# Kernel tuning notes

Hardware: AMD Instinct MI355X
Metric: run time of the kernel (lower is better)

Reference implementation:

```python
import jax, jax.numpy as jnp
import numpy as np

NUM_HEADS = 4
NUM_POINTS = 8


def setup_inputs() -> dict:
    key0 = jax.random.key(0)
    ks = jax.random.split(key0, 14)
    B, S, N, D, C = 1, 6, 10000, 4, 128
    Hf, Wf = 46, 80
    M = Hf * Wf
    HP2 = NUM_HEADS * NUM_POINTS * 2
    HP = NUM_HEADS * NUM_POINTS
    inp = {
        "query": jax.random.normal(ks[0], (B, N, C), jnp.float32),
        "key": jax.random.normal(ks[1], (S, M, B, C), jnp.float32),
        "value": jax.random.normal(ks[2], (S, M, B, C), jnp.float32),
        "query_pos": jax.random.normal(ks[3], (B, N, C), jnp.float32),
        "reference_points_cam": jax.random.uniform(ks[4], (S, B, N, D, 2), jnp.float32),
        "Wv": jax.random.normal(ks[5], (C, C), jnp.float32) * 0.02,
        "bv": jnp.zeros((C,), jnp.float32),
        "Wo": jax.random.normal(ks[6], (C, HP2), jnp.float32) * 0.02,
        "bo": jax.random.normal(ks[7], (HP2,), jnp.float32) * 0.5,
        "Wa": jax.random.normal(ks[8], (C, HP), jnp.float32) * 0.02,
        "ba": jnp.zeros((HP,), jnp.float32),
        "Wp": jax.random.normal(ks[9], (C, C), jnp.float32) * 0.02,
        "bp": jnp.zeros((C,), jnp.float32),
        "spatial_shapes": np.array([[Hf, Wf]], dtype=np.int64),
        "bev_mask": jax.random.uniform(ks[10], (S, B, N, D)) < 0.3,
    }
    return inp


def _bilinear_sample(value_hw, loc, Hf, Wf):
    # value_hw: [BS, H, Hf*Wf, Dh]; loc: [BS, L, H, P, 2] normalized to [0,1]
    # grid_sample(align_corners=False, padding=zeros) semantics: ix = x*W - 0.5
    x = loc[..., 0] * Wf - 0.5
    y = loc[..., 1] * Hf - 0.5
    x0 = jnp.floor(x)
    y0 = jnp.floor(y)
    lx = x - x0
    ly = y - y0
    x0i = x0.astype(jnp.int32)
    y0i = y0.astype(jnp.int32)

    BS, L, H, P = x.shape
    Dh = value_hw.shape[-1]

    def gat(xi, yi):
        valid = (xi >= 0) & (xi < Wf) & (yi >= 0) & (yi < Hf)
        idx = jnp.clip(yi, 0, Hf - 1) * Wf + jnp.clip(xi, 0, Wf - 1)  # [BS,L,H,P]
        idx_t = idx.transpose(0, 2, 1, 3).reshape(BS, H, L * P)
        v = jnp.take_along_axis(value_hw, idx_t[..., None], axis=2)  # [BS,H,L*P,Dh]
        v = v.reshape(BS, H, L, P, Dh)
        return v * valid.transpose(0, 2, 1, 3)[..., None]

    def wt(w):  # [BS,L,H,P] -> [BS,H,L,P,1]
        return w.transpose(0, 2, 1, 3)[..., None]

    out = (gat(x0i, y0i) * wt((1 - lx) * (1 - ly))
           + gat(x0i + 1, y0i) * wt(lx * (1 - ly))
           + gat(x0i, y0i + 1) * wt((1 - lx) * ly)
           + gat(x0i + 1, y0i + 1) * wt(lx * ly))
    return out  # [BS,H,L,P,Dh]


def _deform_attn(q, val, ref, Hf, Wf, Wv, bv, Wo, bo, Wa, ba):
    # q: [BS,L,C], val: [BS,M,C], ref: [BS,L,D,2]
    BS, L, C = q.shape
    Dh = C // NUM_HEADS
    D = ref.shape[2]
    value_p = (val @ Wv + bv).reshape(BS, -1, NUM_HEADS, Dh)
    value_hw = value_p.transpose(0, 2, 1, 3)  # [BS,H,M,Dh]

    off = (q @ Wo + bo).reshape(BS, L, NUM_HEADS, NUM_POINTS, 2)
    attw = jax.nn.softmax((q @ Wa + ba).reshape(BS, L, NUM_HEADS, NUM_POINTS), axis=-1)

    normalizer = jnp.array([Wf, Hf], dtype=q.dtype)  # (x_norm, y_norm)
    off = off / normalizer
    # split points into (points_per_Z, num_Z_anchors) and add per-anchor reference
    off = off.reshape(BS, L, NUM_HEADS, NUM_POINTS // D, D, 2)
    loc = ref[:, :, None, None, :, :] + off  # [BS,L,H,P//D,D,2]
    loc = loc.reshape(BS, L, NUM_HEADS, NUM_POINTS, 2)

    sampled = _bilinear_sample(value_hw, loc, Hf, Wf)  # [BS,H,L,P,Dh]
    out = jnp.einsum('bhlpd,blhp->blhd', sampled, attw)
    return out.reshape(BS, L, C)


def reference(query, key, value, query_pos, reference_points_cam,
              Wv, bv, Wo, bo, Wa, ba, Wp, bp, spatial_shapes, bev_mask):
    B, N, C = query.shape
    S, M = key.shape[0], key.shape[1]
    Hf = int(spatial_shapes[0][0])
    Wf = int(spatial_shapes[0][1])

    q = query + query_pos
    # dense equivalent of the per-camera nonzero() rebatch: run deformable
    # attention for every (batch, camera, query), then mask + scatter-add.
    q_bs = jnp.broadcast_to(q[:, None], (B, S, N, C)).reshape(B * S, N, C)
    ref_bs = reference_points_cam.transpose(1, 0, 2, 3, 4).reshape(B * S, N, -1, 2)
    val_bs = value.transpose(2, 0, 1, 3).reshape(B * S, M, C)

    out = _deform_attn(q_bs, val_bs, ref_bs, Hf, Wf, Wv, bv, Wo, bo, Wa, ba)
    out = out.reshape(B, S, N, C)

    mask_q = (bev_mask.sum(-1) > 0)            # [S,B,N] query visible in camera
    mask_q = mask_q.transpose(1, 0, 2)         # [B,S,N]
    slots = jnp.einsum('bsnc,bsn->bnc', out, mask_q.astype(out.dtype))
    count = jnp.maximum(mask_q.sum(1).astype(out.dtype), 1.0)  # [B,N]
    slots = slots / count[..., None]
    # dropout in eval mode is identity
    return slots @ Wp + bp + query
```

## Files before the change

### kernel.cpp

```cpp
#include <hip/hip_runtime.h>


#define S_DIM 6
#define N_DIM 10000
#define C_DIM 128
#define M_DIM 3680
#define H_DIM 4
#define P_DIM 8
#define DH    32
#define HF    46
#define WF    80

#define G_Q   4
#define NENT  (S_DIM * P_DIM * H_DIM)
#define VHW_SHORTS (S_DIM * H_DIM * M_DIM * DH)

__device__ __forceinline__ float bfl(unsigned u) { return __uint_as_float(u << 16); }
__device__ __forceinline__ float bfh(unsigned u) { return __uint_as_float(u & 0xffff0000u); }
__device__ __forceinline__ unsigned short f2bf(float f) {
    unsigned b = __float_as_uint(f);
    b += 0x7FFFu + ((b >> 16) & 1u);
    return (unsigned short)(b >> 16);
}

__global__ __launch_bounds__(256) void vproj_kernel(
    const float* __restrict__ value,
    const float* __restrict__ Wv,
    const float* __restrict__ bv,
    unsigned short* __restrict__ vhw)
{
    const int row0 = blockIdx.x * 32;
    const int t = threadIdx.x;
    const int tc = t & 31, tr = t >> 5;
    const int c0 = tc * 4, r0 = tr * 4;
    __shared__ float vs[32][C_DIM];

    for (int i = t; i < 32 * 32; i += 256) {
        const int row = i >> 5, c4 = (i & 31) * 4;
        *(float4*)&vs[row][c4] =
            *(const float4*)&value[(size_t)(row0 + row) * C_DIM + c4];
    }
    __syncthreads();

    float acc[4][4];
#pragma unroll
    for (int r = 0; r < 4; ++r)
#pragma unroll
        for (int c = 0; c < 4; ++c) acc[r][c] = 0.f;

    for (int k = 0; k < C_DIM; k += 4) {
        const float4 w0 = *(const float4*)&Wv[(k + 0) * C_DIM + c0];
        const float4 w1 = *(const float4*)&Wv[(k + 1) * C_DIM + c0];
        const float4 w2 = *(const float4*)&Wv[(k + 2) * C_DIM + c0];
        const float4 w3 = *(const float4*)&Wv[(k + 3) * C_DIM + c0];
#pragma unroll
        for (int r = 0; r < 4; ++r) {
            const float4 v = *(const float4*)&vs[r0 + r][k];
            acc[r][0] = fmaf(v.x, w0.x, acc[r][0]);
            acc[r][0] = fmaf(v.y, w1.x, acc[r][0]);
            acc[r][0] = fmaf(v.z, w2.x, acc[r][0]);
            acc[r][0] = fmaf(v.w, w3.x, acc[r][0]);
            acc[r][1] = fmaf(v.x, w0.y, acc[r][1]);
            acc[r][1] = fmaf(v.y, w1.y, acc[r][1]);
            acc[r][1] = fmaf(v.z, w2.y, acc[r][1]);
            acc[r][1] = fmaf(v.w, w3.y, acc[r][1]);
            acc[r][2] = fmaf(v.x, w0.z, acc[r][2]);
            acc[r][2] = fmaf(v.y, w1.z, acc[r][2]);
            acc[r][2] = fmaf(v.z, w2.z, acc[r][2]);
            acc[r][2] = fmaf(v.w, w3.z, acc[r][2]);
            acc[r][3] = fmaf(v.x, w0.w, acc[r][3]);
            acc[r][3] = fmaf(v.y, w1.w, acc[r][3]);
            acc[r][3] = fmaf(v.z, w2.w, acc[r][3]);
            acc[r][3] = fmaf(v.w, w3.w, acc[r][3]);
        }
    }

    const float4 bb = *(const float4*)&bv[c0];
    const int h = c0 >> 5, dh0 = c0 & 31;
#pragma unroll
    for (int r = 0; r < 4; ++r) {
        const int row = row0 + r0 + r;
        const int s = row / M_DIM, m = row - s * M_DIM;
        ushort4 o;
        o.x = f2bf(acc[r][0] + bb.x);
        o.y = f2bf(acc[r][1] + bb.y);
        o.z = f2bf(acc[r][2] + bb.z);
        o.w = f2bf(acc[r][3] + bb.w);
        *(ushort4*)&vhw[(((size_t)s * H_DIM + h) * M_DIM + m) * DH + dh0] = o;
    }
}

__global__ __launch_bounds__(256, 4) void attn_kernel(
    const unsigned short* __restrict__ vhw,
    const float* __restrict__ query,
    const float* __restrict__ query_pos,
    const float* __restrict__ Wo, const float* __restrict__ bo,
    const float* __restrict__ Wa, const float* __restrict__ ba,
    const float* __restrict__ refpts,
    const void* __restrict__ bev_mask,
    const void* __restrict__ sshapes,
    const float* __restrict__ Wp, const float* __restrict__ bp,
    float* __restrict__ out)
{
    const int n0 = blockIdx.x * G_Q;
    const int t = threadIdx.x;

    __shared__ float  qs[G_Q][C_DIM];
    __shared__ float  s_offr[G_Q][64];
    __shared__ float  s_ar[G_Q][32];
    __shared__ float  s_attw[G_Q][32];
    __shared__ int4   s_o[G_Q][S_DIM][P_DIM][H_DIM];
    __shared__ float4 s_w[G_Q][S_DIM][P_DIM][H_DIM];
    __shared__ float  s_slots[G_Q][C_DIM];
    __shared__ int    s_mask[G_Q][S_DIM];
    __shared__ float  s_inv[G_Q];

    for (int i = t; i < G_Q * C_DIM; i += 256) {
        const int g = i >> 7, c = i & 127;
        const size_t a = (size_t)(n0 + g) * C_DIM + c;
        qs[g][c] = query[a] + query_pos[a];
    }
    if (t < G_Q * S_DIM) {
        const int g = t / S_DIM, s = t - g * S_DIM;
        const int n = n0 + g;
        const int* ss32 = (const int*)sshapes;
        const bool i32mode = (ss32[1] == WF);
        int mk;
        if (i32mode) {
            const int* bm = (const int*)bev_mask + ((size_t)s * N_DIM + n) * 4;
            mk = (bm[0] | bm[1] | bm[2] | bm[3]) ? 1 : 0;
        } else {
            const unsigned char* bm =
                (const unsigned char*)bev_mask + ((size_t)s * N_DIM + n) * 4;
            mk = (bm[0] | bm[1] | bm[2] | bm[3]) ? 1 : 0;
        }
        s_mask[g][s] = mk;
    }
    __syncthreads();
    if (t < G_Q) {
        int c = 0;
#pragma unroll
        for (int s = 0; s < S_DIM; ++s) c += s_mask[t][s];
        s_inv[t] = 1.f / fmaxf((float)c, 1.f);
    }

    {
        const int g = t >> 6, j = t & 63;
        float acc = 0.f;
        for (int k = 0; k < C_DIM; k += 4) {
            const float4 q4 = *(const float4*)&qs[g][k];
            acc = fmaf(q4.x, Wo[(k + 0) * 64 + j], acc);
            acc = fmaf(q4.y, Wo[(k + 1) * 64 + j], acc);
            acc = fmaf(q4.z, Wo[(k + 2) * 64 + j], acc);
            acc = fmaf(q4.w, Wo[(k + 3) * 64 + j], acc);
        }
        s_offr[g][j] = acc + bo[j];
    }
    if (t < G_Q * 32) {
        const int g = t >> 5, jj = t & 31;
        float acc = 0.f;
        for (int k = 0; k < C_DIM; k += 4) {
            const float4 q4 = *(const float4*)&qs[g][k];
            acc = fmaf(q4.x, Wa[(k + 0) * 32 + jj], acc);
            acc = fmaf(q4.y, Wa[(k + 1) * 32 + jj], acc);
            acc = fmaf(q4.z, Wa[(k + 2) * 32 + jj], acc);
            acc = fmaf(q4.w, Wa[(k + 3) * 32 + jj], acc);
        }
        s_ar[g][jj] = acc + ba[jj];
    }
    __syncthreads();
    if (t < G_Q * 32) {
        const int g = t >> 5, hp = t & 31;
        const float v = s_ar[g][hp];
        float m = v;
        for (int d = 1; d < 8; d <<= 1) m = fmaxf(m, __shfl_xor(m, d, 8));
        const float e = expf(v - m);
        float sum = e;
        for (int d = 1; d < 8; d <<= 1) sum += __shfl_xor(sum, d, 8);
        s_attw[g][hp] = e / sum;
    }
    __syncthreads();

    for (int i = t; i < G_Q * NENT; i += 256) {
        const int g = i / NENT;
        const int e = i - g * NENT;
        const int s = e >> 5;
        const int rem = e & 31;
        const int p = rem >> 2, h = rem & 3;
        const int hp = h * P_DIM + p;
        const int d = p & 3;
        const int n = n0 + g;

        const float aw = s_attw[g][hp];
        const float offx = s_offr[g][hp * 2 + 0] / (float)WF;
        const float offy = s_offr[g][hp * 2 + 1] / (float)HF;
        const float refx = refpts[(((size_t)s * N_DIM + n) * 4 + d) * 2 + 0];
        const float refy = refpts[(((size_t)s * N_DIM + n) * 4 + d) * 2 + 1];

        const float x = (refx + offx) * (float)WF - 0.5f;
        const float y = (refy + offy) * (float)HF - 0.5f;
        const float x0f = floorf(x), y0f = floorf(y);
        const float lx = x - x0f, ly = y - y0f;
        const int x0 = (int)x0f, y0 = (int)y0f;
        const int x1 = x0 + 1, y1 = y0 + 1;

        const bool vx0 = (x0 >= 0) & (x0 < WF);
        const bool vx1 = (x1 >= 0) & (x1 < WF);
        const bool vy0 = (y0 >= 0) & (y0 < HF);
        const bool vy1 = (y1 >= 0) & (y1 < HF);

        const int cx0 = min(max(x0, 0), WF - 1);
        const int cx1 = min(max(x1, 0), WF - 1);
        const int cy0 = min(max(y0, 0), HF - 1);
        const int cy1 = min(max(y1, 0), HF - 1);

        const int base = (s * H_DIM + h) * M_DIM;
        const int r0 = base + cy0 * WF;
        const int r1 = base + cy1 * WF;
        s_o[g][s][p][h] = make_int4((r0 + cx0) * (DH * 2),
                                    (r0 + cx1) * (DH * 2),
                                    (r1 + cx0) * (DH * 2),
                                    (r1 + cx1) * (DH * 2));

        const float wx0 = 1.f - lx, wy0 = 1.f - ly;
        s_w[g][s][p][h] = make_float4((vx0 & vy0) ? wx0 * wy0 * aw : 0.f,
                                      (vx1 & vy0) ? lx  * wy0 * aw : 0.f,
                                      (vx0 & vy1) ? wx0 * ly  * aw : 0.f,
                                      (vx1 & vy1) ? lx  * ly  * aw : 0.f);
    }
    __syncthreads();

    {
        const char* vb = (const char*)vhw;
        const int g = t >> 6;
        const int lane = t & 63;
        const int h = lane >> 4;
        const int dhp4 = (lane & 15) * 4;
        float accx = 0.f, accy = 0.f;

        for (int s = 0; s < S_DIM; ++s) {
            if (!s_mask[g][s]) continue;
#pragma unroll
            for (int pg = 0; pg < 4; ++pg) {
                const int4 o0 = s_o[g][s][pg * 2 + 0][h];
                const int4 o1 = s_o[g][s][pg * 2 + 1][h];
                unsigned u0 = *(const unsigned*)(vb + (o0.x + dhp4));
                unsigned u1 = *(const unsigned*)(vb + (o0.y + dhp4));
                unsigned u2 = *(const unsigned*)(vb + (o0.z + dhp4));
                unsigned u3 = *(const unsigned*)(vb + (o0.w + dhp4));
                unsigned u4 = *(const unsigned*)(vb + (o1.x + dhp4));
                unsigned u5 = *(const unsigned*)(vb + (o1.y + dhp4));
                unsigned u6 = *(const unsigned*)(vb + (o1.z + dhp4));
                unsigned u7 = *(const unsigned*)(vb + (o1.w + dhp4));
                const float4 w0 = s_w[g][s][pg * 2 + 0][h];
                const float4 w1 = s_w[g][s][pg * 2 + 1][h];
                accx = fmaf(w0.x, bfl(u0), accx); accy = fmaf(w0.x, bfh(u0), accy);
                accx = fmaf(w0.y, bfl(u1), accx); accy = fmaf(w0.y, bfh(u1), accy);
                accx = fmaf(w0.z, bfl(u2), accx); accy = fmaf(w0.z, bfh(u2), accy);
                accx = fmaf(w0.w, bfl(u3), accx); accy = fmaf(w0.w, bfh(u3), accy);
                accx = fmaf(w1.x, bfl(u4), accx); accy = fmaf(w1.x, bfh(u4), accy);
                accx = fmaf(w1.y, bfl(u5), accx); accy = fmaf(w1.y, bfh(u5), accy);
                accx = fmaf(w1.z, bfl(u6), accx); accy = fmaf(w1.z, bfh(u6), accy);
                accx = fmaf(w1.w, bfl(u7), accx); accy = fmaf(w1.w, bfh(u7), accy);
            }
        }
        const float inv = s_inv[g];
        *(float2*)&s_slots[g][h * 32 + (lane & 15) * 2] =
            make_float2(accx * inv, accy * inv);
    }
    __syncthreads();

    {
        const int c = t & 127, half = t >> 7;
        const int g0 = half * 2;
        float a0 = 0.f, a1 = 0.f;
        for (int k = 0; k < C_DIM; k += 4) {
            const float4 s0 = *(const float4*)&s_slots[g0][k];
            const float4 s1 = *(const float4*)&s_slots[g0 + 1][k];
            const float w0 = Wp[(k + 0) * C_DIM + c];
            const float w1 = Wp[(k + 1) * C_DIM + c];
            const float w2 = Wp[(k + 2) * C_DIM + c];
            const float w3 = Wp[(k + 3) * C_DIM + c];
            a0 = fmaf(s0.x, w0, a0); a1 = fmaf(s1.x, w0, a1);
            a0 = fmaf(s0.y, w1, a0); a1 = fmaf(s1.y, w1, a1);
            a0 = fmaf(s0.z, w2, a0); a1 = fmaf(s1.z, w2, a1);
            a0 = fmaf(s0.w, w3, a0); a1 = fmaf(s1.w, w3, a1);
        }
        const int na = n0 + g0;
        const float bb = bp[c];
        out[(size_t)na * C_DIM + c]       = a0 + bb + query[(size_t)na * C_DIM + c];
        out[(size_t)(na + 1) * C_DIM + c] = a1 + bb + query[(size_t)(na + 1) * C_DIM + c];
    }
}

extern "C" void kernel_launch(void* const* d_in, const int* in_sizes, int n_in,
                              void* d_out, int out_size, void* d_ws, size_t ws_size,
                              hipStream_t stream) {
    const float* query     = (const float*)d_in[0];
    const float* value     = (const float*)d_in[2];
    const float* query_pos = (const float*)d_in[3];
    const float* refpts    = (const float*)d_in[4];
    const float* Wv        = (const float*)d_in[5];
    const float* bv        = (const float*)d_in[6];
    const float* Wo        = (const float*)d_in[7];
    const float* bo        = (const float*)d_in[8];
    const float* Wa        = (const float*)d_in[9];
    const float* ba        = (const float*)d_in[10];
    const float* Wp        = (const float*)d_in[11];
    const float* bp        = (const float*)d_in[12];
    const void*  sshapes   = d_in[13];
    const void*  bev_mask  = d_in[14];

    unsigned short* vhw = (unsigned short*)d_ws;
    float* outp = (float*)d_out;

    hipLaunchKernelGGL(vproj_kernel, dim3((S_DIM * M_DIM) / 32), dim3(256), 0, stream,
                       value, Wv, bv, vhw);
    hipLaunchKernelGGL(attn_kernel, dim3(N_DIM / G_Q), dim3(256), 0, stream,
                       vhw, query, query_pos, Wo, bo, Wa, ba,
                       refpts, bev_mask, sshapes, Wp, bp, outp);
}
```

Before: 78.27 us.

## Pack sample pixel indices and bilinear weights into 16-bit fields, raise occupancy

Sampling offsets are now stored as 16-bit pixel indices and the bilinear weights as bf16 pairs, halving the shared-memory footprint of the per-sample tables. The gather loop rebuilds byte offsets with shifts and masks from a per-camera base. The softmax is fused into the Wa projection, which removes one barrier and the s_ar buffer. Launch bounds are raised to 8 blocks per SM to allow more waves in flight. The cost is extra ALU work for unpacking, tighter register limits, and bf16 rounding of the sampling weights.

```diff
diff --git a/kernel.cpp b/kernel.cpp
--- a/kernel.cpp
+++ b/kernel.cpp
@@ -90,7 +90,7 @@
     }
 }
 
-__global__ __launch_bounds__(256, 4) void attn_kernel(
+__global__ __launch_bounds__(256, 8) void attn_kernel(
     const unsigned short* __restrict__ vhw,
     const float* __restrict__ query,
     const float* __restrict__ query_pos,
@@ -107,10 +107,9 @@
 
     __shared__ float  qs[G_Q][C_DIM];
     __shared__ float  s_offr[G_Q][64];
-    __shared__ float  s_ar[G_Q][32];
     __shared__ float  s_attw[G_Q][32];
-    __shared__ int4   s_o[G_Q][S_DIM][P_DIM][H_DIM];
-    __shared__ float4 s_w[G_Q][S_DIM][P_DIM][H_DIM];
+    __shared__ uint2  s_pixd[G_Q][S_DIM][P_DIM][H_DIM];
+    __shared__ uint2  s_wbd[G_Q][S_DIM][P_DIM][H_DIM];
     __shared__ float  s_slots[G_Q][C_DIM];
     __shared__ int    s_mask[G_Q][S_DIM];
     __shared__ float  s_inv[G_Q];
@@ -158,26 +157,21 @@
     }
     if (t < G_Q * 32) {
         const int g = t >> 5, jj = t & 31;
-        float acc = 0.f;
+        float ar = 0.f;
         for (int k = 0; k < C_DIM; k += 4) {
             const float4 q4 = *(const float4*)&qs[g][k];
-            acc = fmaf(q4.x, Wa[(k + 0) * 32 + jj], acc);
-            acc = fmaf(q4.y, Wa[(k + 1) * 32 + jj], acc);
-            acc = fmaf(q4.z, Wa[(k + 2) * 32 + jj], acc);
-            acc = fmaf(q4.w, Wa[(k + 3) * 32 + jj], acc);
-        }
-        s_ar[g][jj] = acc + ba[jj];
-    }
-    __syncthreads();
-    if (t < G_Q * 32) {
-        const int g = t >> 5, hp = t & 31;
-        const float v = s_ar[g][hp];
-        float m = v;
+            ar = fmaf(q4.x, Wa[(k + 0) * 32 + jj], ar);
+            ar = fmaf(q4.y, Wa[(k + 1) * 32 + jj], ar);
+            ar = fmaf(q4.z, Wa[(k + 2) * 32 + jj], ar);
+            ar = fmaf(q4.w, Wa[(k + 3) * 32 + jj], ar);
+        }
+        ar += ba[jj];
+        float m = ar;
         for (int d = 1; d < 8; d <<= 1) m = fmaxf(m, __shfl_xor(m, d, 8));
-        const float e = expf(v - m);
+        const float e = expf(ar - m);
         float sum = e;
         for (int d = 1; d < 8; d <<= 1) sum += __shfl_xor(sum, d, 8);
-        s_attw[g][hp] = e / sum;
+        s_attw[g][jj] = e / sum;
     }
     __syncthreads();
 
@@ -209,24 +203,25 @@
         const bool vy0 = (y0 >= 0) & (y0 < HF);
         const bool vy1 = (y1 >= 0) & (y1 < HF);
 
-        const int cx0 = min(max(x0, 0), WF - 1);
-        const int cx1 = min(max(x1, 0), WF - 1);
-        const int cy0 = min(max(y0, 0), HF - 1);
-        const int cy1 = min(max(y1, 0), HF - 1);
-
-        const int base = (s * H_DIM + h) * M_DIM;
-        const int r0 = base + cy0 * WF;
-        const int r1 = base + cy1 * WF;
-        s_o[g][s][p][h] = make_int4((r0 + cx0) * (DH * 2),
-                                    (r0 + cx1) * (DH * 2),
-                                    (r1 + cx0) * (DH * 2),
-                                    (r1 + cx1) * (DH * 2));
+        const unsigned cx0 = (unsigned)min(max(x0, 0), WF - 1);
+        const unsigned cx1 = (unsigned)min(max(x1, 0), WF - 1);
+        const unsigned cy0 = (unsigned)min(max(y0, 0), HF - 1);
+        const unsigned cy1 = (unsigned)min(max(y1, 0), HF - 1);
+
+        const unsigned p00 = cy0 * WF + cx0;
+        const unsigned p10 = cy0 * WF + cx1;
+        const unsigned p01 = cy1 * WF + cx0;
+        const unsigned p11 = cy1 * WF + cx1;
+        s_pixd[g][s][p][h] = make_uint2(p00 | (p10 << 16), p01 | (p11 << 16));
 
         const float wx0 = 1.f - lx, wy0 = 1.f - ly;
-        s_w[g][s][p][h] = make_float4((vx0 & vy0) ? wx0 * wy0 * aw : 0.f,
-                                      (vx1 & vy0) ? lx  * wy0 * aw : 0.f,
-                                      (vx0 & vy1) ? wx0 * ly  * aw : 0.f,
-                                      (vx1 & vy1) ? lx  * ly  * aw : 0.f);
+        const float w00 = (vx0 & vy0) ? wx0 * wy0 * aw : 0.f;
+        const float w10 = (vx1 & vy0) ? lx  * wy0 * aw : 0.f;
+        const float w01 = (vx0 & vy1) ? wx0 * ly  * aw : 0.f;
+        const float w11 = (vx1 & vy1) ? lx  * ly  * aw : 0.f;
+        s_wbd[g][s][p][h] = make_uint2(
+            (unsigned)f2bf(w00) | ((unsigned)f2bf(w10) << 16),
+            (unsigned)f2bf(w01) | ((unsigned)f2bf(w11) << 16));
     }
     __syncthreads();
 
@@ -240,28 +235,33 @@
 
         for (int s = 0; s < S_DIM; ++s) {
             if (!s_mask[g][s]) continue;
+            const int sb = ((s * H_DIM + h) * M_DIM) * (DH * 2) + dhp4;
 #pragma unroll
             for (int pg = 0; pg < 4; ++pg) {
-                const int4 o0 = s_o[g][s][pg * 2 + 0][h];
-                const int4 o1 = s_o[g][s][pg * 2 + 1][h];
-                unsigned u0 = *(const unsigned*)(vb + (o0.x + dhp4));
-                unsigned u1 = *(const unsigned*)(vb + (o0.y + dhp4));
-                unsigned u2 = *(const unsigned*)(vb + (o0.z + dhp4));
-                unsigned u3 = *(const unsigned*)(vb + (o0.w + dhp4));
-                unsigned u4 = *(const unsigned*)(vb + (o1.x + dhp4));
-                unsigned u5 = *(const unsigned*)(vb + (o1.y + dhp4));
-                unsigned u6 = *(const unsigned*)(vb + (o1.z + dhp4));
-                unsigned u7 = *(const unsigned*)(vb + (o1.w + dhp4));
-                const float4 w0 = s_w[g][s][pg * 2 + 0][h];
-                const float4 w1 = s_w[g][s][pg * 2 + 1][h];
-                accx = fmaf(w0.x, bfl(u0), accx); accy = fmaf(w0.x, bfh(u0), accy);
-                accx = fmaf(w0.y, bfl(u1), accx); accy = fmaf(w0.y, bfh(u1), accy);
-                accx = fmaf(w0.z, bfl(u2), accx); accy = fmaf(w0.z, bfh(u2), accy);
-                accx = fmaf(w0.w, bfl(u3), accx); accy = fmaf(w0.w, bfh(u3), accy);
-                accx = fmaf(w1.x, bfl(u4), accx); accy = fmaf(w1.x, bfh(u4), accy);
-                accx = fmaf(w1.y, bfl(u5), accx); accy = fmaf(w1.y, bfh(u5), accy);
-                accx = fmaf(w1.z, bfl(u6), accx); accy = fmaf(w1.z, bfh(u6), accy);
-                accx = fmaf(w1.w, bfl(u7), accx); accy = fmaf(w1.w, bfh(u7), accy);
+                const uint2 pa = s_pixd[g][s][pg * 2 + 0][h];
+                const uint2 pb = s_pixd[g][s][pg * 2 + 1][h];
+                const unsigned u0 = *(const unsigned*)(vb + (sb + (int)((pa.x <<  6) & 0x3fffc0u)));
+                const unsigned u1 = *(const unsigned*)(vb + (sb + (int)((pa.x >> 10) & 0x3fffc0u)));
+                const unsigned u2 = *(const unsigned*)(vb + (sb + (int)((pa.y <<  6) & 0x3fffc0u)));
+                const unsigned u3 = *(const unsigned*)(vb + (sb + (int)((pa.y >> 10) & 0x3fffc0u)));
+                const unsigned u4 = *(const unsigned*)(vb + (sb + (int)((pb.x <<  6) & 0x3fffc0u)));
+                const unsigned u5 = *(const unsigned*)(vb + (sb + (int)((pb.x >> 10) & 0x3fffc0u)));
+                const unsigned u6 = *(const unsigned*)(vb + (sb + (int)((pb.y <<  6) & 0x3fffc0u)));
+                const unsigned u7 = *(const unsigned*)(vb + (sb + (int)((pb.y >> 10) & 0x3fffc0u)));
+                const uint2 wa = s_wbd[g][s][pg * 2 + 0][h];
+                const uint2 wb2 = s_wbd[g][s][pg * 2 + 1][h];
+                const float w00 = bfl(wa.x),  w10 = bfh(wa.x);
+                const float w01 = bfl(wa.y),  w11 = bfh(wa.y);
+                const float x00 = bfl(wb2.x), x10 = bfh(wb2.x);
+                const float x01 = bfl(wb2.y), x11 = bfh(wb2.y);
+                accx = fmaf(w00, bfl(u0), accx); accy = fmaf(w00, bfh(u0), accy);
+                accx = fmaf(w10, bfl(u1), accx); accy = fmaf(w10, bfh(u1), accy);
+                accx = fmaf(w01, bfl(u2), accx); accy = fmaf(w01, bfh(u2), accy);
+                accx = fmaf(w11, bfl(u3), accx); accy = fmaf(w11, bfh(u3), accy);
+                accx = fmaf(x00, bfl(u4), accx); accy = fmaf(x00, bfh(u4), accy);
+                accx = fmaf(x10, bfl(u5), accx); accy = fmaf(x10, bfh(u5), accy);
+                accx = fmaf(x01, bfl(u6), accx); accy = fmaf(x01, bfh(u6), accy);
+                accx = fmaf(x11, bfl(u7), accx); accy = fmaf(x11, bfh(u7), accy);
             }
         }
         const float inv = s_inv[g];
```

Result: slower. 82.30 us (+5.2%).
